# Kernel tuning notes

Hardware: AMD Instinct MI355X
Metric: run time of the kernel (lower is better)

## Reference

```python
import jax, jax.numpy as jnp
import numpy as np

C = 256
POOL = 4

def setup_inputs() -> dict:
    key = jax.random.key(0)
    ks = jax.random.split(key, 8)
    B, H, W = 4, 256, 256
    d = C // 8
    x = jax.random.normal(ks[0], (B, C, H, W), dtype=jnp.float32)
    # 1x1 conv weights stored as [out, in] matrices (kernel_size=1)
    s = 1.0 / np.sqrt(C)
    Wq = jax.random.uniform(ks[1], (d, C), jnp.float32, -s, s)
    bq = jax.random.uniform(ks[2], (d,), jnp.float32, -s, s)
    Wk = jax.random.uniform(ks[3], (d, C), jnp.float32, -s, s)
    bk = jax.random.uniform(ks[4], (d,), jnp.float32, -s, s)
    Wv = jax.random.uniform(ks[5], (C, C), jnp.float32, -s, s)
    bv = jax.random.uniform(ks[6], (C,), jnp.float32, -s, s)
    gamma = jax.random.normal(ks[7], (1,), jnp.float32) * 0.1
    return {"x": x, "Wq": Wq, "bq": bq, "Wk": Wk, "bk": bk,
            "Wv": Wv, "bv": bv, "gamma": gamma}


def reference(x, Wq, bq, Wk, bk, Wv, bv, gamma):
    B, Cc, H, W = x.shape
    Hp, Wp = H // POOL, W // POOL
    # AvgPool2d(kernel=4, stride=4)
    xp = x.reshape(B, Cc, Hp, POOL, Wp, POOL).mean(axis=(3, 5))  # [B,C,Hp,Wp]
    xf = xp.reshape(B, Cc, Hp * Wp)                              # [B,C,N]
    # 1x1 convs == channel matmuls
    q = jnp.einsum('dc,bcn->bdn', Wq, xf) + bq[None, :, None]    # [B,d,N]
    k = jnp.einsum('dc,bcn->bdn', Wk, xf) + bk[None, :, None]    # [B,d,N]
    v = jnp.einsum('ec,bcn->ben', Wv, xf) + bv[None, :, None]    # [B,C,N]
    # energy[b,n,m] = q[:, :, n] . k[:, :, m]
    energy = jnp.einsum('bdn,bdm->bnm', q, k)                    # [B,N,N]
    attn = jax.nn.softmax(energy, axis=-1)
    # out = v @ attn^T  -> out[b,c,n] = sum_m v[b,c,m] * attn[b,n,m]
    out = jnp.einsum('bcm,bnm->bcn', v, attn)                    # [B,C,N]
    out = out.reshape(B, Cc, Hp, Wp)
    # bilinear upsample, half-pixel centers (align_corners=False)
    up = jax.image.resize(out, (B, Cc, H, W), method='bilinear')
    return gamma[0] * up + x
```

## Files before the change

kernel.cpp:

```cpp
#include <hip/hip_runtime.h>

#define B_ 4
#define C_ 256
#define N_ 4096
#define D_ 32

typedef __bf16 bf16;
typedef __bf16 bf16x4 __attribute__((ext_vector_type(4)));
typedef __bf16 bf16x8 __attribute__((ext_vector_type(8)));
typedef float f32x4 __attribute__((ext_vector_type(4)));

__global__ __launch_bounds__(256) void k_prep(
    const float* __restrict__ Wq, const float* __restrict__ bq,
    const float* __restrict__ Wk, const float* __restrict__ bk,
    const float* __restrict__ Wv, const float* __restrict__ bv,
    bf16* __restrict__ wt, float* __restrict__ bias) {
  int r = blockIdx.x, t = threadIdx.x;
  const float* src; float bval;
  if (r < 32)      { src = Wq + (r << 8);        bval = bq[r]; }
  else if (r < 64) { src = Wk + ((r - 32) << 8); bval = bk[r - 32]; }
  else             { src = Wv + ((r - 64) << 8); bval = bv[r - 64]; }
  wt[(r << 8) + t] = (bf16)src[t];
  if (t == 0) bias[r] = bval;
}

__global__ __launch_bounds__(512) void k_fused(const float* __restrict__ x,
    const bf16* __restrict__ wt, const float* __restrict__ bias,
    bf16* __restrict__ qt, bf16* __restrict__ kt, bf16* __restrict__ v) {
  __shared__ bf16 xsb[64][264];
  int tid = threadIdx.x, wave = tid >> 6, l = tid & 63;
  int lg = l >> 4, ll = l & 15;
  int b = blockIdx.x >> 6, hp = blockIdx.x & 63, n0 = hp * 64;

  const float4* x4 = reinterpret_cast<const float4*>(x) +
      ((size_t)((b * 256 + wave * 32) * 256 + hp * 4)) * 64 + l;
  for (int c0 = 0; c0 < 32; c0 += 4) {
    float s[4] = {0.f, 0.f, 0.f, 0.f};
    #pragma unroll
    for (int j = 0; j < 4; ++j) {
      const float4* p = x4 + (size_t)(c0 + j) * 16384;
      #pragma unroll
      for (int dh = 0; dh < 4; ++dh) {
        float4 a = p[dh * 64];
        s[j] += a.x + a.y + a.z + a.w;
      }
    }
    bf16x4 pk;
    #pragma unroll
    for (int j = 0; j < 4; ++j) pk[j] = (bf16)(s[j] * 0.0625f);
    *reinterpret_cast<bf16x4*>(&xsb[l][wave * 32 + c0]) = pk;
  }
  __syncthreads();

  f32x4 acc[3][4];
  #pragma unroll
  for (int j = 0; j < 3; ++j)
    #pragma unroll
    for (int cb = 0; cb < 4; ++cb) acc[j][cb] = (f32x4){0.f, 0.f, 0.f, 0.f};

  for (int kk = 0; kk < 8; ++kk) {
    bf16x8 bfr[4];
    #pragma unroll
    for (int cb = 0; cb < 4; ++cb)
      bfr[cb] = *reinterpret_cast<const bf16x8*>(&xsb[cb * 16 + ll][kk * 32 + lg * 8]);
    #pragma unroll
    for (int j = 0; j < 3; ++j) {
      int rb = wave + j * 8;
      if (rb < 20) {
        bf16x8 afr = *reinterpret_cast<const bf16x8*>(
            wt + ((size_t)(rb * 16 + ll)) * 256 + kk * 32 + lg * 8);
        #pragma unroll
        for (int cb = 0; cb < 4; ++cb)
          acc[j][cb] = __builtin_amdgcn_mfma_f32_16x16x32_bf16(afr, bfr[cb], acc[j][cb], 0, 0, 0);
      }
    }
  }

  #pragma unroll
  for (int j = 0; j < 3; ++j) {
    int rb = wave + j * 8;
    if (rb < 20) {
      int row0 = rb * 16 + lg * 4;
      float4 b4 = *reinterpret_cast<const float4*>(bias + row0);
      #pragma unroll
      for (int cb = 0; cb < 4; ++cb) {
        int n = n0 + cb * 16 + ll;
        float v0 = acc[j][cb][0] + b4.x, v1 = acc[j][cb][1] + b4.y;
        float v2 = acc[j][cb][2] + b4.z, v3 = acc[j][cb][3] + b4.w;
        if (row0 < 32) {
          bf16x4 pk = {(bf16)v0, (bf16)v1, (bf16)v2, (bf16)v3};
          *reinterpret_cast<bf16x4*>(qt + ((size_t)(b * N_ + n)) * D_ + row0) = pk;
        } else if (row0 < 64) {
          bf16x4 pk = {(bf16)v0, (bf16)v1, (bf16)v2, (bf16)v3};
          *reinterpret_cast<bf16x4*>(kt + ((size_t)(b * N_ + n)) * D_ + row0 - 32) = pk;
        } else {
          int c = row0 - 64;
          v[((size_t)(b * 256 + c + 0)) * N_ + n] = (bf16)v0;
          v[((size_t)(b * 256 + c + 1)) * N_ + n] = (bf16)v1;
          v[((size_t)(b * 256 + c + 2)) * N_ + n] = (bf16)v2;
          v[((size_t)(b * 256 + c + 3)) * N_ + n] = (bf16)v3;
        }
      }
    }
  }
}

__global__ __launch_bounds__(512) void k_attn(const bf16* __restrict__ qt,
    const bf16* __restrict__ kt, const bf16* __restrict__ v,
    float* __restrict__ outs) {
  __shared__ bf16 p_s[32][264];
  __shared__ float l_red[8][32];
  __shared__ float l_s[32];
  int tid = threadIdx.x, wave = tid >> 6, l = tid & 63;
  int lg = l >> 4, ll = l & 15;
  int blk = blockIdx.x;
  int b  = (blk & 7) >> 1;
  int nt = ((blk >> 3) << 1) | (blk & 1);
  int n0 = nt * 32;

  const f32x4 fz = {0.f, 0.f, 0.f, 0.f};

  bf16x8 aq[2];
  #pragma unroll
  for (int tnf = 0; tnf < 2; ++tnf)
    aq[tnf] = *reinterpret_cast<const bf16x8*>(
        qt + ((size_t)(b * N_ + n0 + tnf * 16 + ll)) * D_ + lg * 8);

  f32x4 acc[2][2];
  float lsum[2][4];
  #pragma unroll
  for (int a = 0; a < 2; ++a) {
    #pragma unroll
    for (int cf = 0; cf < 2; ++cf) acc[a][cf] = fz;
    #pragma unroll
    for (int r = 0; r < 4; ++r) lsum[a][r] = 0.f;
  }

  const int mw = wave * 32;
  const int cw = wave * 32;

  for (int t = 0; t < 16; ++t) {
    int m0 = t * 256;
    #pragma unroll
    for (int tmf = 0; tmf < 2; ++tmf) {
      int mglob = m0 + mw + tmf * 16 + ll;
      bf16x8 bk8 = *reinterpret_cast<const bf16x8*>(
          kt + ((size_t)(b * N_ + mglob)) * D_ + lg * 8);
      #pragma unroll
      for (int tnf = 0; tnf < 2; ++tnf) {
        f32x4 e = __builtin_amdgcn_mfma_f32_16x16x32_bf16(aq[tnf], bk8, fz, 0, 0, 0);
        int col = mw + tmf * 16 + ll;
        #pragma unroll
        for (int r = 0; r < 4; ++r) {
          float p = __expf(e[r]);
          lsum[tnf][r] += p;
          p_s[tnf * 16 + lg * 4 + r][col] = (bf16)p;
        }
      }
    }
    __syncthreads();
    #pragma unroll
    for (int kk = 0; kk < 8; ++kk) {
      bf16x8 pa[2];
      #pragma unroll
      for (int tnf = 0; tnf < 2; ++tnf)
        pa[tnf] = *reinterpret_cast<const bf16x8*>(
            &p_s[tnf * 16 + ll][kk * 32 + lg * 8]);
      #pragma unroll
      for (int cf = 0; cf < 2; ++cf) {
        int c = cw + cf * 16 + ll;
        bf16x8 bv8 = *reinterpret_cast<const bf16x8*>(
            v + ((size_t)((b << 8) + c)) * N_ + m0 + kk * 32 + lg * 8);
        acc[0][cf] = __builtin_amdgcn_mfma_f32_16x16x32_bf16(pa[0], bv8, acc[0][cf], 0, 0, 0);
        acc[1][cf] = __builtin_amdgcn_mfma_f32_16x16x32_bf16(pa[1], bv8, acc[1][cf], 0, 0, 0);
      }
    }
    __syncthreads();
  }

  #pragma unroll
  for (int tnf = 0; tnf < 2; ++tnf) {
    #pragma unroll
    for (int r = 0; r < 4; ++r) {
      float s = lsum[tnf][r];
      s += __shfl_xor(s, 1);
      s += __shfl_xor(s, 2);
      s += __shfl_xor(s, 4);
      s += __shfl_xor(s, 8);
      if (ll == 0) l_red[wave][tnf * 16 + lg * 4 + r] = s;
    }
  }
  __syncthreads();
  if (tid < 32) {
    float s = 0.f;
    #pragma unroll
    for (int w = 0; w < 8; ++w) s += l_red[w][tid];
    l_s[tid] = s;
  }
  __syncthreads();

  #pragma unroll
  for (int tnf = 0; tnf < 2; ++tnf) {
    #pragma unroll
    for (int r = 0; r < 4; ++r) {
      int tn = tnf * 16 + lg * 4 + r;
      float inv = 1.0f / l_s[tn];
      #pragma unroll
      for (int cf = 0; cf < 2; ++cf) {
        int c = cw + cf * 16 + ll;
        outs[((size_t)((b << 8) + c)) * N_ + n0 + tn] = acc[tnf][cf][r] * inv;
      }
    }
  }
}

__global__ __launch_bounds__(256) void k_up(const float* __restrict__ outs,
    const float* __restrict__ x, const float* __restrict__ gamma,
    float* __restrict__ out) {
  int j = blockIdx.x * 256 + threadIdx.x;
  int wq = j & 63, h = (j >> 6) & 255, bc = j >> 14;
  int th = 2 * h - 3;
  int h0 = th < 0 ? -1 : (th >> 3);
  float fh = (float)(th - 8 * h0) * 0.125f;
  int i0h = h0 < 0 ? 0 : h0;
  int i1h = h0 + 1 > 63 ? 63 : h0 + 1;
  const float* s0 = outs + ((size_t)(bc * 64 + i0h)) * 64;
  const float* s1 = outs + ((size_t)(bc * 64 + i1h)) * 64;
  float g = gamma[0];
  float r4[4];
  #pragma unroll
  for (int k2 = 0; k2 < 4; ++k2) {
    int w = wq * 4 + k2;
    int tw = 2 * w - 3;
    int w0 = tw < 0 ? -1 : (tw >> 3);
    float fw = (float)(tw - 8 * w0) * 0.125f;
    int i0 = w0 < 0 ? 0 : w0;
    int i1 = w0 + 1 > 63 ? 63 : w0 + 1;
    float a = s0[i0], bb = s0[i1], cc = s1[i0], dd = s1[i1];
    float top = a + fw * (bb - a);
    float bot = cc + fw * (dd - cc);
    r4[k2] = top + fh * (bot - top);
  }
  size_t o4 = (size_t)(bc * 256 + h) * 64 + wq;
  float4 xv = reinterpret_cast<const float4*>(x)[o4];
  float4 o;
  o.x = g * r4[0] + xv.x; o.y = g * r4[1] + xv.y;
  o.z = g * r4[2] + xv.z; o.w = g * r4[3] + xv.w;
  reinterpret_cast<float4*>(out)[o4] = o;
}

extern "C" void kernel_launch(void* const* d_in, const int* in_sizes, int n_in,
                              void* d_out, int out_size, void* d_ws, size_t ws_size,
                              hipStream_t stream) {
  const float* x     = (const float*)d_in[0];
  const float* Wq    = (const float*)d_in[1];
  const float* bq    = (const float*)d_in[2];
  const float* Wk    = (const float*)d_in[3];
  const float* bk    = (const float*)d_in[4];
  const float* Wv    = (const float*)d_in[5];
  const float* bv    = (const float*)d_in[6];
  const float* gamma = (const float*)d_in[7];
  float* out = (float*)d_out;

  char* ws = (char*)d_ws;
  float* outs = (float*)(ws);
  bf16*  v    = (bf16*) (ws + (16u << 20));
  bf16*  qt   = (bf16*) (ws + (24u << 20));
  bf16*  kt   = (bf16*) (ws + (25u << 20));
  bf16*  wt   = (bf16*) (ws + (26u << 20));
  float* bias = (float*)(ws + (27u << 20));

  hipLaunchKernelGGL(k_prep,  dim3(320),   dim3(256), 0, stream,
                     Wq, bq, Wk, bk, Wv, bv, wt, bias);
  hipLaunchKernelGGL(k_fused, dim3(256),   dim3(512), 0, stream,
                     x, wt, bias, qt, kt, v);
  hipLaunchKernelGGL(k_attn,  dim3(512),   dim3(512), 0, stream, qt, kt, v, outs);
  hipLaunchKernelGGL(k_up,    dim3(65536), dim3(256), 0, stream, outs, x, gamma, out);
}
```

Before: 298.2 us.

## Use 1024-thread blocks for projection and attention, stage upsample source in LDS

Result: faster. 259.6 us (-13.0%).

```diff
diff --git a/kernel.cpp b/kernel.cpp
--- a/kernel.cpp
+++ b/kernel.cpp
@@ -24,7 +24,7 @@
   if (t == 0) bias[r] = bval;
 }
 
-__global__ __launch_bounds__(512) void k_fused(const float* __restrict__ x,
+__global__ __launch_bounds__(1024) void k_fused(const float* __restrict__ x,
     const bf16* __restrict__ wt, const float* __restrict__ bias,
     bf16* __restrict__ qt, bf16* __restrict__ kt, bf16* __restrict__ v) {
   __shared__ bf16 xsb[64][264];
@@ -33,8 +33,8 @@
   int b = blockIdx.x >> 6, hp = blockIdx.x & 63, n0 = hp * 64;
 
   const float4* x4 = reinterpret_cast<const float4*>(x) +
-      ((size_t)((b * 256 + wave * 32) * 256 + hp * 4)) * 64 + l;
-  for (int c0 = 0; c0 < 32; c0 += 4) {
+      ((size_t)((b * 256 + wave * 16) * 256 + hp * 4)) * 64 + l;
+  for (int c0 = 0; c0 < 16; c0 += 4) {
     float s[4] = {0.f, 0.f, 0.f, 0.f};
     #pragma unroll
     for (int j = 0; j < 4; ++j) {
@@ -48,13 +48,13 @@
     bf16x4 pk;
     #pragma unroll
     for (int j = 0; j < 4; ++j) pk[j] = (bf16)(s[j] * 0.0625f);
-    *reinterpret_cast<bf16x4*>(&xsb[l][wave * 32 + c0]) = pk;
-  }
-  __syncthreads();
-
-  f32x4 acc[3][4];
-  #pragma unroll
-  for (int j = 0; j < 3; ++j)
+    *reinterpret_cast<bf16x4*>(&xsb[l][wave * 16 + c0]) = pk;
+  }
+  __syncthreads();
+
+  f32x4 acc[2][4];
+  #pragma unroll
+  for (int j = 0; j < 2; ++j)
     #pragma unroll
     for (int cb = 0; cb < 4; ++cb) acc[j][cb] = (f32x4){0.f, 0.f, 0.f, 0.f};
 
@@ -64,8 +64,8 @@
     for (int cb = 0; cb < 4; ++cb)
       bfr[cb] = *reinterpret_cast<const bf16x8*>(&xsb[cb * 16 + ll][kk * 32 + lg * 8]);
     #pragma unroll
-    for (int j = 0; j < 3; ++j) {
-      int rb = wave + j * 8;
+    for (int j = 0; j < 2; ++j) {
+      int rb = wave + j * 16;
       if (rb < 20) {
         bf16x8 afr = *reinterpret_cast<const bf16x8*>(
             wt + ((size_t)(rb * 16 + ll)) * 256 + kk * 32 + lg * 8);
@@ -77,8 +77,8 @@
   }
 
   #pragma unroll
-  for (int j = 0; j < 3; ++j) {
-    int rb = wave + j * 8;
+  for (int j = 0; j < 2; ++j) {
+    int rb = wave + j * 16;
     if (rb < 20) {
       int row0 = rb * 16 + lg * 4;
       float4 b4 = *reinterpret_cast<const float4*>(bias + row0);
@@ -105,51 +105,47 @@
   }
 }
 
-__global__ __launch_bounds__(512) void k_attn(const bf16* __restrict__ qt,
+__global__ __launch_bounds__(1024) void k_attn(const bf16* __restrict__ qt,
     const bf16* __restrict__ kt, const bf16* __restrict__ v,
     float* __restrict__ outs) {
-  __shared__ bf16 p_s[32][264];
-  __shared__ float l_red[8][32];
-  __shared__ float l_s[32];
+  __shared__ bf16 p_s[64][264];
+  __shared__ float l_red[16][64];
+  __shared__ float l_s[64];
   int tid = threadIdx.x, wave = tid >> 6, l = tid & 63;
   int lg = l >> 4, ll = l & 15;
   int blk = blockIdx.x;
   int b  = (blk & 7) >> 1;
   int nt = ((blk >> 3) << 1) | (blk & 1);
-  int n0 = nt * 32;
+  int n0 = nt * 64;
 
   const f32x4 fz = {0.f, 0.f, 0.f, 0.f};
 
-  bf16x8 aq[2];
-  #pragma unroll
-  for (int tnf = 0; tnf < 2; ++tnf)
+  bf16x8 aq[4];
+  #pragma unroll
+  for (int tnf = 0; tnf < 4; ++tnf)
     aq[tnf] = *reinterpret_cast<const bf16x8*>(
         qt + ((size_t)(b * N_ + n0 + tnf * 16 + ll)) * D_ + lg * 8);
 
-  f32x4 acc[2][2];
-  float lsum[2][4];
-  #pragma unroll
-  for (int a = 0; a < 2; ++a) {
-    #pragma unroll
-    for (int cf = 0; cf < 2; ++cf) acc[a][cf] = fz;
+  f32x4 acc[4];
+  float lsum[4][4];
+  #pragma unroll
+  for (int a = 0; a < 4; ++a) {
+    acc[a] = fz;
     #pragma unroll
     for (int r = 0; r < 4; ++r) lsum[a][r] = 0.f;
   }
 
-  const int mw = wave * 32;
-  const int cw = wave * 32;
-
+  const int mw = wave * 16;
   for (int t = 0; t < 16; ++t) {
     int m0 = t * 256;
-    #pragma unroll
-    for (int tmf = 0; tmf < 2; ++tmf) {
-      int mglob = m0 + mw + tmf * 16 + ll;
+    {
+      int mglob = m0 + mw + ll;
       bf16x8 bk8 = *reinterpret_cast<const bf16x8*>(
           kt + ((size_t)(b * N_ + mglob)) * D_ + lg * 8);
       #pragma unroll
-      for (int tnf = 0; tnf < 2; ++tnf) {
+      for (int tnf = 0; tnf < 4; ++tnf) {
         f32x4 e = __builtin_amdgcn_mfma_f32_16x16x32_bf16(aq[tnf], bk8, fz, 0, 0, 0);
-        int col = mw + tmf * 16 + ll;
+        int col = mw + ll;
         #pragma unroll
         for (int r = 0; r < 4; ++r) {
           float p = __expf(e[r]);
@@ -161,25 +157,20 @@
     __syncthreads();
     #pragma unroll
     for (int kk = 0; kk < 8; ++kk) {
-      bf16x8 pa[2];
-      #pragma unroll
-      for (int tnf = 0; tnf < 2; ++tnf)
-        pa[tnf] = *reinterpret_cast<const bf16x8*>(
+      bf16x8 bv8 = *reinterpret_cast<const bf16x8*>(
+          v + ((size_t)((b << 8) + mw + ll)) * N_ + m0 + kk * 32 + lg * 8);
+      #pragma unroll
+      for (int tnf = 0; tnf < 4; ++tnf) {
+        bf16x8 pa = *reinterpret_cast<const bf16x8*>(
             &p_s[tnf * 16 + ll][kk * 32 + lg * 8]);
-      #pragma unroll
-      for (int cf = 0; cf < 2; ++cf) {
-        int c = cw + cf * 16 + ll;
-        bf16x8 bv8 = *reinterpret_cast<const bf16x8*>(
-            v + ((size_t)((b << 8) + c)) * N_ + m0 + kk * 32 + lg * 8);
-        acc[0][cf] = __builtin_amdgcn_mfma_f32_16x16x32_bf16(pa[0], bv8, acc[0][cf], 0, 0, 0);
-        acc[1][cf] = __builtin_amdgcn_mfma_f32_16x16x32_bf16(pa[1], bv8, acc[1][cf], 0, 0, 0);
+        acc[tnf] = __builtin_amdgcn_mfma_f32_16x16x32_bf16(pa, bv8, acc[tnf], 0, 0, 0);
       }
     }
     __syncthreads();
   }
 
   #pragma unroll
-  for (int tnf = 0; tnf < 2; ++tnf) {
+  for (int tnf = 0; tnf < 4; ++tnf) {
     #pragma unroll
     for (int r = 0; r < 4; ++r) {
       float s = lsum[tnf][r];
@@ -191,62 +182,70 @@
     }
   }
   __syncthreads();
-  if (tid < 32) {
+  if (tid < 64) {
     float s = 0.f;
     #pragma unroll
-    for (int w = 0; w < 8; ++w) s += l_red[w][tid];
+    for (int w = 0; w < 16; ++w) s += l_red[w][tid];
     l_s[tid] = s;
   }
   __syncthreads();
 
-  #pragma unroll
-  for (int tnf = 0; tnf < 2; ++tnf) {
-    #pragma unroll
-    for (int r = 0; r < 4; ++r) {
-      int tn = tnf * 16 + lg * 4 + r;
-      float inv = 1.0f / l_s[tn];
-      #pragma unroll
-      for (int cf = 0; cf < 2; ++cf) {
-        int c = cw + cf * 16 + ll;
-        outs[((size_t)((b << 8) + c)) * N_ + n0 + tn] = acc[tnf][cf][r] * inv;
-      }
-    }
+  int c = mw + ll;
+  #pragma unroll
+  for (int tnf = 0; tnf < 4; ++tnf) {
+    int tn0 = tnf * 16 + lg * 4;
+    float4 o;
+    o.x = acc[tnf][0] / l_s[tn0 + 0];
+    o.y = acc[tnf][1] / l_s[tn0 + 1];
+    o.z = acc[tnf][2] / l_s[tn0 + 2];
+    o.w = acc[tnf][3] / l_s[tn0 + 3];
+    *reinterpret_cast<float4*>(outs + ((size_t)((b << 8) + c)) * N_ + n0 + tn0) = o;
   }
 }
 
 __global__ __launch_bounds__(256) void k_up(const float* __restrict__ outs,
     const float* __restrict__ x, const float* __restrict__ gamma,
     float* __restrict__ out) {
-  int j = blockIdx.x * 256 + threadIdx.x;
-  int wq = j & 63, h = (j >> 6) & 255, bc = j >> 14;
-  int th = 2 * h - 3;
-  int h0 = th < 0 ? -1 : (th >> 3);
-  float fh = (float)(th - 8 * h0) * 0.125f;
-  int i0h = h0 < 0 ? 0 : h0;
-  int i1h = h0 + 1 > 63 ? 63 : h0 + 1;
-  const float* s0 = outs + ((size_t)(bc * 64 + i0h)) * 64;
-  const float* s1 = outs + ((size_t)(bc * 64 + i1h)) * 64;
+  __shared__ float s_o[4096];
+  int tid = threadIdx.x, wave = tid >> 6, tw = tid & 63;
+  int bc = blockIdx.x;
+  const float* src = outs + (size_t)bc * 4096;
+  #pragma unroll
+  for (int ch = 0; ch < 4; ++ch)
+    *reinterpret_cast<float4*>(&s_o[ch * 1024 + tid * 4]) =
+        *reinterpret_cast<const float4*>(src + ch * 1024 + tid * 4);
+  __syncthreads();
+
   float g = gamma[0];
-  float r4[4];
-  #pragma unroll
-  for (int k2 = 0; k2 < 4; ++k2) {
-    int w = wq * 4 + k2;
-    int tw = 2 * w - 3;
-    int w0 = tw < 0 ? -1 : (tw >> 3);
-    float fw = (float)(tw - 8 * w0) * 0.125f;
-    int i0 = w0 < 0 ? 0 : w0;
-    int i1 = w0 + 1 > 63 ? 63 : w0 + 1;
-    float a = s0[i0], bb = s0[i1], cc = s1[i0], dd = s1[i1];
-    float top = a + fw * (bb - a);
-    float bot = cc + fw * (dd - cc);
-    r4[k2] = top + fh * (bot - top);
-  }
-  size_t o4 = (size_t)(bc * 256 + h) * 64 + wq;
-  float4 xv = reinterpret_cast<const float4*>(x)[o4];
-  float4 o;
-  o.x = g * r4[0] + xv.x; o.y = g * r4[1] + xv.y;
-  o.z = g * r4[2] + xv.z; o.w = g * r4[3] + xv.w;
-  reinterpret_cast<float4*>(out)[o4] = o;
+  const float4* xr = reinterpret_cast<const float4*>(x) + (size_t)bc * 16384;
+  float4* outr = reinterpret_cast<float4*>(out) + (size_t)bc * 16384;
+
+  int twm = tw == 0 ? 0 : tw - 1;
+  int twp = tw == 63 ? 63 : tw + 1;
+
+  for (int hb = 0; hb < 64; ++hb) {
+    int h = hb * 4 + wave;
+    int th = 2 * h - 3;
+    int h0 = th < 0 ? -1 : (th >> 3);
+    float fh = (float)(th - 8 * h0) * 0.125f;
+    int i0h = h0 < 0 ? 0 : h0;
+    int i1h = h0 + 1 > 63 ? 63 : h0 + 1;
+    const float* r0 = &s_o[i0h * 64];
+    const float* r1 = &s_o[i1h * 64];
+    float a_m = r0[twm], a_c = r0[tw], a_p = r0[twp];
+    float b_m = r1[twm], b_c = r1[tw], b_p = r1[twp];
+    float t0 = a_m + 0.625f * (a_c - a_m), u0 = b_m + 0.625f * (b_c - b_m);
+    float t1 = a_m + 0.875f * (a_c - a_m), u1 = b_m + 0.875f * (b_c - b_m);
+    float t2 = a_c + 0.125f * (a_p - a_c), u2 = b_c + 0.125f * (b_p - b_c);
+    float t3 = a_c + 0.375f * (a_p - a_c), u3 = b_c + 0.375f * (b_p - b_c);
+    float4 xv = xr[h * 64 + tw];
+    float4 o;
+    o.x = g * (t0 + fh * (u0 - t0)) + xv.x;
+    o.y = g * (t1 + fh * (u1 - t1)) + xv.y;
+    o.z = g * (t2 + fh * (u2 - t2)) + xv.z;
+    o.w = g * (t3 + fh * (u3 - t3)) + xv.w;
+    outr[h * 64 + tw] = o;
+  }
 }
 
 extern "C" void kernel_launch(void* const* d_in, const int* in_sizes, int n_in,
@@ -270,10 +269,10 @@
   bf16*  wt   = (bf16*) (ws + (26u << 20));
   float* bias = (float*)(ws + (27u << 20));
 
-  hipLaunchKernelGGL(k_prep,  dim3(320),   dim3(256), 0, stream,
+  hipLaunchKernelGGL(k_prep,  dim3(320),  dim3(256),  0, stream,
                      Wq, bq, Wk, bk, Wv, bv, wt, bias);
-  hipLaunchKernelGGL(k_fused, dim3(256),   dim3(512), 0, stream,
+  hipLaunchKernelGGL(k_fused, dim3(256),  dim3(1024), 0, stream,
                      x, wt, bias, qt, kt, v);
-  hipLaunchKernelGGL(k_attn,  dim3(512),   dim3(512), 0, stream, qt, kt, v, outs);
-  hipLaunchKernelGGL(k_up,    dim3(65536), dim3(256), 0, stream, outs, x, gamma, out);
-}
+  hipLaunchKernelGGL(k_attn,  dim3(256),  dim3(1024), 0, stream, qt, kt, v, outs);
+  hipLaunchKernelGGL(k_up,    dim3(1024), dim3(256),  0, stream, outs, x, gamma, out);
+}
```
